# Kernel tuning notes

Measured on AMD Instinct MI355X. Metric: run time of the kernel, lower is better.

The kernel has to match this reference:

```python
import jax, jax.numpy as jnp
import numpy as np
import math

P_PARTICLES = 50
N_ITERS = 30
ROT_RANGE = math.radians(45.0)
TR_RANGE = 1.0
F_DE = 0.8
CR_DE = 0.9
SUB = 128


def axis_angle_to_rotation_matrix(v):
    # v: [..., 3] axis-angle -> [..., 3, 3] via Rodrigues formula
    theta = jnp.linalg.norm(v, axis=-1, keepdims=True)            # [..., 1]
    k = v / jnp.maximum(theta, 1e-8)
    kx, ky, kz = k[..., 0], k[..., 1], k[..., 2]
    zero = jnp.zeros_like(kx)
    K = jnp.stack([zero, -kz, ky,
                   kz, zero, -kx,
                   -ky, kx, zero], axis=-1).reshape(v.shape[:-1] + (3, 3))
    I = jnp.eye(3, dtype=v.dtype)
    s = jnp.sin(theta)[..., None]
    c = jnp.cos(theta)[..., None]
    R = I + s * K + (1.0 - c) * (K @ K)
    return jnp.where(theta[..., None] < 1e-8, I, R)


def _evaluate(src, tgt, pop):
    # src: [B,S,3] subsampled source, tgt: [B,S,3], pop: [B,P,6]
    R = axis_angle_to_rotation_matrix(pop[..., :3])               # [B,P,3,3]
    t = pop[..., 3:]                                              # [B,P,3]
    # transformed[b,p,n,k] = sum_j src[b,n,j] * R[b,p,k,j] + t[b,p,k]
    x = jnp.einsum('bnj,bpkj->bpnk', src, R) + t[:, :, None, :]   # [B,P,S,3]
    # squared-distance chamfer (symmetric, mean of nearest-neighbor dists)
    xn = jnp.sum(x * x, axis=-1)                                  # [B,P,S]
    yn = jnp.sum(tgt * tgt, axis=-1)                              # [B,S]
    cross = jnp.einsum('bpnd,bmd->bpnm', x, tgt)                  # [B,P,S,S]
    d2 = jnp.maximum(xn[..., None] + yn[:, None, None, :] - 2.0 * cross, 0.0)
    return d2.min(axis=-1).mean(axis=-1) + d2.min(axis=-2).mean(axis=-1)  # [B,P]


def setup_inputs() -> dict:
    key = jax.random.key(0)
    k1, k2 = jax.random.split(key)
    source = jax.random.normal(k1, (32, 16384, 3), dtype=jnp.float32)
    target = jax.random.normal(k2, (32, 16384, 3), dtype=jnp.float32)
    return {"source": source, "target": target}


def reference(source, target):
    B, N, _ = source.shape
    M = target.shape[1]
    P = P_PARTICLES
    key = jax.random.key(42)
    k0, k1, k2, k3, kloop = jax.random.split(key, 5)

    # subsample points for fitness evaluation (shared indices across batch)
    idx_s = jax.random.permutation(k0, N)[:SUB]
    idx_t = jax.random.permutation(k1, M)[:SUB]
    src = source[:, idx_s, :]                                     # [B,S,3]
    tgt = target[:, idx_t, :]                                     # [B,S,3]

    # init population: uniform axis-angle + translation; particle 0 = identity
    rot = jax.random.uniform(k2, (B, P, 3), minval=-ROT_RANGE, maxval=ROT_RANGE)
    tr = jax.random.uniform(k3, (B, P, 3), minval=-TR_RANGE, maxval=TR_RANGE)
    pop = jnp.concatenate([rot, tr], axis=-1).at[:, 0, :].set(0.0)
    fit = _evaluate(src, tgt, pop)                                # [B,P]

    dim_ids = jnp.arange(6)

    def step(carry, k):
        pop, fit = carry
        ka, kb, kc = jax.random.split(k, 3)
        # per-batch random permutations of particle indices (r1, r2, r3)
        perm_keys = jax.random.split(ka, 3 * B)
        perms = jax.vmap(lambda kk: jax.random.permutation(kk, P))(perm_keys)
        perms = perms.reshape(3, B, P)

        def gather(r):
            return jnp.take_along_axis(pop, r[..., None], axis=1)  # [B,P,6]

        x1, x2, x3 = gather(perms[0]), gather(perms[1]), gather(perms[2])
        mutant = x1 + F_DE * (x2 - x3)
        mutant = jnp.concatenate([
            jnp.clip(mutant[..., :3], -ROT_RANGE, ROT_RANGE),
            jnp.clip(mutant[..., 3:], -TR_RANGE, TR_RANGE),
        ], axis=-1)

        rmask = jax.random.uniform(kb, (B, P, 6)) < CR_DE
        j_rand = jax.random.randint(kc, (B, P), 0, 6)
        cross_mask = rmask | (dim_ids == j_rand[..., None])
        trial = jnp.where(cross_mask, mutant, pop)

        tfit = _evaluate(src, tgt, trial)
        improved = tfit < fit
        pop = jnp.where(improved[..., None], trial, pop)
        fit = jnp.where(improved, tfit, fit)
        return (pop, fit), None

    (pop, fit), _ = jax.lax.scan(step, (pop, fit), jax.random.split(kloop, N_ITERS))

    best_idx = jnp.argmin(fit, axis=1)                            # [B]
    best_pos = pop[jnp.arange(B), best_idx]                       # [B,6]
    R_best = axis_angle_to_rotation_matrix(best_pos[:, :3])       # [B,3,3]
    t_best = best_pos[:, 3:]                                      # [B,3]
    aligned = jnp.einsum('bnj,bkj->bnk', source, R_best) + t_best[:, None, :]
    return (R_best, t_best, aligned)
```

## Files before the change

kernel.cpp:

```cpp
#include <hip/hip_runtime.h>
#include <stdint.h>

struct U2 { unsigned a, b; };

__device__ __forceinline__ unsigned rotl32(unsigned v, int r) {
  return (v << r) | (v >> (32 - r));
}

__device__ __forceinline__ U2 tf(U2 k, unsigned x0, unsigned x1) {
  unsigned ks0 = k.a, ks1 = k.b, ks2 = k.a ^ k.b ^ 0x1BD11BDAu;
  x0 += ks0; x1 += ks1;
#define TFG(RA, RB, RC, RD, KA, KB, INC)                  \
  x0 += x1; x1 = rotl32(x1, RA); x1 ^= x0;                \
  x0 += x1; x1 = rotl32(x1, RB); x1 ^= x0;                \
  x0 += x1; x1 = rotl32(x1, RC); x1 ^= x0;                \
  x0 += x1; x1 = rotl32(x1, RD); x1 ^= x0;                \
  x0 += KA; x1 += KB + INC;
  TFG(13, 15, 26, 6, ks1, ks2, 1u)
  TFG(17, 29, 16, 24, ks2, ks0, 2u)
  TFG(13, 15, 26, 6, ks0, ks1, 3u)
  TFG(17, 29, 16, 24, ks1, ks2, 4u)
  TFG(13, 15, 26, 6, ks2, ks0, 5u)
#undef TFG
  U2 r; r.a = x0; r.b = x1; return r;
}

__device__ __forceinline__ U2 split_key(U2 key, int num, int j) {
  (void)num;
  return tf(key, 0u, (unsigned)j);
}
__device__ __forceinline__ unsigned random_bits(U2 key, int n, unsigned e) {
  (void)n;
  U2 r = tf(key, 0u, e);
  return r.a ^ r.b;
}

__device__ __forceinline__ U2 root_key() { U2 k; k.a = 0u; k.b = 42u; return k; }

__device__ __forceinline__ float jax_uniform(U2 key, int n, unsigned e,
                                             float minv, float maxv) {
  unsigned b = random_bits(key, n, e);
  float u = __uint_as_float((b >> 9) | 0x3f800000u) - 1.0f;
  float r = u * (maxv - minv) + minv;
  return fmaxf(minv, r);
}

#define ROTR 0.7853981633974483f
#define SENTINEL 0xFFFFFFFFu

__device__ __forceinline__ void compute_R(float vx, float vy, float vz,
                                          float R[3][3]) {
  float nsq = vx * vx + vy * vy + vz * vz;
  float theta = sqrtf(nsq);
  if (theta < 1e-8f) {
    R[0][0] = 1.f; R[0][1] = 0.f; R[0][2] = 0.f;
    R[1][0] = 0.f; R[1][1] = 1.f; R[1][2] = 0.f;
    R[2][0] = 0.f; R[2][1] = 0.f; R[2][2] = 1.f;
    return;
  }
  float m = fmaxf(theta, 1e-8f);
  float kx = vx / m, ky = vy / m, kz = vz / m;
  float s = sinf(theta), c = cosf(theta);
  float K[3][3] = {{0.f, -kz, ky}, {kz, 0.f, -kx}, {-ky, kx, 0.f}};
  float K2[3][3];
#pragma unroll
  for (int i = 0; i < 3; i++)
#pragma unroll
    for (int j = 0; j < 3; j++)
      K2[i][j] = fmaf(K[i][2], K[2][j], fmaf(K[i][1], K[1][j], K[i][0] * K[0][j]));
  float omc = 1.0f - c;
#pragma unroll
  for (int i = 0; i < 3; i++)
#pragma unroll
    for (int j = 0; j < 3; j++)
      R[i][j] = ((i == j) ? 1.0f : 0.0f) + s * K[i][j] + omc * K2[i][j];
}

__device__ __forceinline__ unsigned long long make_composite(int s, int i) {
  U2 root = root_key();
  U2 kp = split_key(root, 5, s >> 1);
  U2 key;
  if ((s & 1) == 0) {
    key = split_key(kp, 2, 1);
  } else {
    U2 kA = split_key(kp, 2, 0);
    key = split_key(kA, 2, 1);
  }
  unsigned rb = random_bits(key, 16384, (unsigned)i);
  return ((unsigned long long)rb << 32) | (unsigned)i;
}

__device__ __forceinline__ float gload(const float* p) {
  return __hip_atomic_load(const_cast<float*>(p), __ATOMIC_RELAXED,
                           __HIP_MEMORY_SCOPE_AGENT);
}
__device__ __forceinline__ void gstore(float* p, float v) {
  __hip_atomic_store(p, v, __ATOMIC_RELAXED, __HIP_MEMORY_SCOPE_AGENT);
}
__device__ __forceinline__ unsigned uload(const unsigned* p) {
  return __hip_atomic_load(const_cast<unsigned*>(p), __ATOMIC_RELAXED,
                           __HIP_MEMORY_SCOPE_AGENT);
}

__device__ __forceinline__ float poll_word(const float* p) {
  const unsigned* up = (const unsigned*)p;
  unsigned v = uload(up);
  while (v == SENTINEL) v = uload(up);
  return __uint_as_float(v);
}

__global__ __launch_bounds__(256) void hist_kernel(unsigned* __restrict__ hist) {
  int gid = blockIdx.x * 256 + threadIdx.x;
  int s = gid >> 14, i = gid & 16383;
  unsigned long long c = make_composite(s, i);
  unsigned bucket = (unsigned)(c >> 56);
  atomicAdd(&hist[s * 256 + bucket], 1u);
}

__global__ __launch_bounds__(256) void prefix_kernel(
    const unsigned* __restrict__ hist, unsigned* __restrict__ base,
    unsigned* __restrict__ cursor) {
  __shared__ unsigned h[4][256];
  int t = threadIdx.x;
#pragma unroll
  for (int s = 0; s < 4; s++) h[s][t] = hist[s * 256 + t];
  __syncthreads();
#pragma unroll
  for (int s = 0; s < 4; s++) {
    unsigned acc = 0;
    for (int j = 0; j < 256; j++) acc += (j < t) ? h[s][j] : 0u;
    base[s * 256 + t] = acc;
    cursor[s * 256 + t] = acc;
  }
}

__global__ __launch_bounds__(256) void scatterb_kernel(
    unsigned* __restrict__ cursor, unsigned long long* __restrict__ sorted) {
  int gid = blockIdx.x * 256 + threadIdx.x;
  int s = gid >> 14, i = gid & 16383;
  unsigned long long c = make_composite(s, i);
  unsigned bucket = (unsigned)(c >> 56);
  unsigned pos = atomicAdd(&cursor[s * 256 + bucket], 1u);
  sorted[(s << 14) + pos] = c;
}

__global__ __launch_bounds__(256) void rank_kernel(
    const unsigned long long* __restrict__ sorted,
    const unsigned* __restrict__ base, const unsigned* __restrict__ hist,
    unsigned* __restrict__ rank_all, unsigned* __restrict__ x1buf) {
  int gid = blockIdx.x * 256 + threadIdx.x;
  int s = gid >> 14, k = gid & 16383;
  unsigned long long c = sorted[(s << 14) + k];
  unsigned bucket = (unsigned)(c >> 56);
  unsigned b0 = base[s * 256 + bucket];
  unsigned cnt = hist[s * 256 + bucket];
  unsigned less = 0;
  for (unsigned j = 0; j < cnt; j++)
    less += (sorted[(s << 14) + b0 + j] < c) ? 1u : 0u;
  unsigned i = (unsigned)(c & 0xffffffffull);
  unsigned rank = b0 + less;
  if ((s & 1) == 0) x1buf[((s >> 1) << 14) + rank] = i;
  else              rank_all[(s << 14) + i] = rank;
}

__global__ __launch_bounds__(256) void idx_kernel(
    const unsigned* __restrict__ rank_all, const unsigned* __restrict__ x1buf,
    int* __restrict__ idx) {
  int gid = blockIdx.x * 256 + threadIdx.x;
  int perm = gid >> 14, i = gid & 16383;
  unsigned r = rank_all[((perm * 2 + 1) << 14) + i];
  if (r < 128u) idx[perm * 128 + (int)r] = (int)x1buf[(perm << 14) + i];
}

__global__ __launch_bounds__(128) void setupperm_kernel(
    const float* __restrict__ source, const float* __restrict__ target,
    const int* __restrict__ idx, float* __restrict__ src,
    float* __restrict__ tgt, float* __restrict__ yn,
    unsigned* __restrict__ packg) {
  int blk = blockIdx.x;
  int tid = threadIdx.x;
  if (blk < 32) {
    int b = blk;
    int is = idx[tid], it = idx[128 + tid];
#pragma unroll
    for (int d = 0; d < 3; d++)
      src[(b * 128 + tid) * 3 + d] = source[((size_t)b * 16384 + is) * 3 + d];
    float y0 = target[((size_t)b * 16384 + it) * 3 + 0];
    float y1 = target[((size_t)b * 16384 + it) * 3 + 1];
    float y2 = target[((size_t)b * 16384 + it) * 3 + 2];
    tgt[(b * 128 + tid) * 3 + 0] = y0;
    tgt[(b * 128 + tid) * 3 + 1] = y1;
    tgt[(b * 128 + tid) * 3 + 2] = y2;
    yn[b * 128 + tid] = y0 * y0 + y1 * y1 + y2 * y2;
    return;
  }
  int blk2 = blk - 32;
  int it = blk2 >> 5, b = blk2 & 31;
  __shared__ unsigned pbits[3][64];
  __shared__ int lperm[3][64];
  U2 root = root_key();
  U2 kloop = split_key(root, 5, 4);
  U2 kit = split_key(kloop, 30, it);
  U2 ka = split_key(kit, 3, 0);
  for (int e = tid; e < 150; e += 128) {
    int r = e / 50, q = e % 50;
    U2 pk = split_key(ka, 96, r * 32 + b);
    U2 sub = split_key(pk, 2, 1);
    pbits[r][q] = random_bits(sub, 50, (unsigned)q);
  }
  __syncthreads();
  for (int e = tid; e < 150; e += 128) {
    int r = e / 50, q = e % 50;
    unsigned bq = pbits[r][q];
    int cnt = 0;
    for (int j = 0; j < 50; j++) {
      unsigned bj = pbits[r][j];
      cnt += (bj < bq || (bj == bq && j < q)) ? 1 : 0;
    }
    lperm[r][cnt] = q;
  }
  __syncthreads();
  if (tid < 50) {
    int p = tid, bp = b * 50 + p;
    U2 kb = split_key(kit, 3, 1);
    U2 kc = split_key(kit, 3, 2);
    U2 kc1 = split_key(kc, 2, 0), kc2 = split_key(kc, 2, 1);
    unsigned hb = random_bits(kc1, 1600, (unsigned)bp);
    unsigned lb = random_bits(kc2, 1600, (unsigned)bp);
    int jr = (int)((((hb % 6u) * 4u) + (lb % 6u)) % 6u);
    unsigned mask = 0;
#pragma unroll
    for (int d = 0; d < 6; d++) {
      unsigned rb = random_bits(kb, 9600, (unsigned)(bp * 6 + d));
      float u = __uint_as_float((rb >> 9) | 0x3f800000u) - 1.0f;
      if ((u < 0.9f) || (d == jr)) mask |= (1u << d);
    }
    unsigned pack = (unsigned)lperm[0][p] | ((unsigned)lperm[1][p] << 6) |
                    ((unsigned)lperm[2][p] << 12) | (mask << 18);
    packg[(it * 32 + b) * 50 + p] = pack;
  }
}

__device__ __forceinline__ float eval_pose_core(
    float p0, float p1, float p2, float p3, float p4, float p5,
    float s0, float s1, float s2, int tid, const float4* syv, float4* xsv,
    float* rowpart, float* red1, float* red2) {
  float Rm[3][3];
  compute_R(p0, p1, p2, Rm);
  float x0 = fmaf(Rm[0][2], s2, fmaf(Rm[0][1], s1, Rm[0][0] * s0)) + p3;
  float x1 = fmaf(Rm[1][2], s2, fmaf(Rm[1][1], s1, Rm[1][0] * s0)) + p4;
  float x2 = fmaf(Rm[2][2], s2, fmaf(Rm[2][1], s1, Rm[2][0] * s0)) + p5;
  float xn = x0 * x0 + x1 * x1 + x2 * x2;
  xsv[tid] = make_float4(x0, x1, x2, xn);
  __syncthreads();
  int rg = tid & 31, cq = tid >> 5;
  float4 xr0 = xsv[4 * rg + 0];
  float4 xr1 = xsv[4 * rg + 1];
  float4 xr2 = xsv[4 * rg + 2];
  float4 xr3 = xsv[4 * rg + 3];
  float racc0 = 3.402823466e38f, racc1 = 3.402823466e38f;
  float racc2 = 3.402823466e38f, racc3 = 3.402823466e38f;
  float cacc[32];
#pragma unroll
  for (int cj = 0; cj < 32; cj++) {
    float4 y = syv[(cq << 5) + cj];
    float cr0 = fmaf(xr0.z, y.z, fmaf(xr0.y, y.y, xr0.x * y.x));
    float d0 = (xr0.w + y.w) - 2.0f * cr0; d0 = fmaxf(d0, 0.0f);
    float cr1 = fmaf(xr1.z, y.z, fmaf(xr1.y, y.y, xr1.x * y.x));
    float d1 = (xr1.w + y.w) - 2.0f * cr1; d1 = fmaxf(d1, 0.0f);
    float cr2 = fmaf(xr2.z, y.z, fmaf(xr2.y, y.y, xr2.x * y.x));
    float d2_ = (xr2.w + y.w) - 2.0f * cr2; d2_ = fmaxf(d2_, 0.0f);
    float cr3 = fmaf(xr3.z, y.z, fmaf(xr3.y, y.y, xr3.x * y.x));
    float d3 = (xr3.w + y.w) - 2.0f * cr3; d3 = fmaxf(d3, 0.0f);
    racc0 = fminf(racc0, d0); racc1 = fminf(racc1, d1);
    racc2 = fminf(racc2, d2_); racc3 = fminf(racc3, d3);
    cacc[cj] = fminf(fminf(d0, d1), fminf(d2_, d3));
  }
  rowpart[cq * 128 + 4 * rg + 0] = racc0;
  rowpart[cq * 128 + 4 * rg + 1] = racc1;
  rowpart[cq * 128 + 4 * rg + 2] = racc2;
  rowpart[cq * 128 + 4 * rg + 3] = racc3;
#pragma unroll
  for (int m = 16; m >= 1; m >>= 1) {
    bool hi = (rg & m) != 0;
#pragma unroll
    for (int j = 0; j < m; j++) {
      float lo_v = cacc[j], hi_v = cacc[j + m];
      float mine = hi ? hi_v : lo_v;
      float send = hi ? lo_v : hi_v;
      float recv = __shfl_xor(send, m, 64);
      cacc[j] = fminf(mine, recv);
    }
  }
  float colmin = cacc[0];
  __syncthreads();
  float rv = rowpart[tid];
  rv = fminf(rv, rowpart[128 + tid]);
  rv = fminf(rv, rowpart[256 + tid]);
  rv = fminf(rv, rowpart[384 + tid]);
  red1[tid] = rv;
  red2[tid] = colmin;
  __syncthreads();
  int l = tid & 63;
  float v1 = red1[l] + red1[l + 64];
  float v2 = red2[l] + red2[l + 64];
#pragma unroll
  for (int m = 32; m >= 1; m >>= 1) {
    v1 += __shfl_xor(v1, m, 64);
    v2 += __shfl_xor(v2, m, 64);
  }
  return v1 * 0.0078125f + v2 * 0.0078125f;
}

__device__ __forceinline__ float pop0_val(int b, int r, int d) {
  if (r == 0) return 0.0f;
  U2 root = root_key();
  unsigned ridx = (unsigned)((b * 50 + r) * 3 + (d % 3));
  if (d < 3) {
    U2 k2 = split_key(root, 5, 2);
    return jax_uniform(k2, 4800, ridx, -ROTR, ROTR);
  }
  U2 k3 = split_key(root, 5, 3);
  return jax_uniform(k3, 4800, ridx, -1.0f, 1.0f);
}

__global__ __launch_bounds__(128, 4) void de_loop_kernel(
    const float* __restrict__ srcb, const float* __restrict__ tgtb,
    const float* __restrict__ ynb, const unsigned* __restrict__ packg,
    float* __restrict__ estate, const float* __restrict__ source,
    float* __restrict__ out) {
  int blk = blockIdx.x;
  int b = blk / 50, p = blk % 50;
  int bp = blk;
  int tid = threadIdx.x;
  __shared__ float strial[8];
  __shared__ float pv4[4][6];
  __shared__ float4 syv[128];
  __shared__ float4 xsv[128];
  __shared__ float rowpart[512];
  __shared__ float red1[128];
  __shared__ float red2[128];
  __shared__ float fl[52];
  __shared__ float Rsh2[12];

  {
    float y0 = tgtb[(b * 128 + tid) * 3 + 0];
    float y1 = tgtb[(b * 128 + tid) * 3 + 1];
    float y2 = tgtb[(b * 128 + tid) * 3 + 2];
    syv[tid] = make_float4(y0, y1, y2, ynb[b * 128 + tid]);
  }
  float s0 = srcb[(b * 128 + tid) * 3 + 0];
  float s1 = srcb[(b * 128 + tid) * 3 + 1];
  float s2 = srcb[(b * 128 + tid) * 3 + 2];

  float own_f = 0.0f;
  float own_e = 0.0f;

  unsigned pack_next = packg[(0 * 32 + b) * 50 + p];

  for (int it = 0; it < 30; it++) {
    unsigned pack = pack_next;
    if (it < 29) pack_next = packg[((it + 1) * 32 + b) * 50 + p];
    int i1 = (int)(pack & 63u);
    int i2 = (int)((pack >> 6) & 63u);
    int i3 = (int)((pack >> 12) & 63u);
    unsigned mask = (pack >> 18) & 63u;

    if (it == 0) {
      if (tid < 24) {
        int u = tid / 6, d = tid % 6;
        int rows[4] = {p, i1, i2, i3};
        pv4[u][d] = pop0_val(b, rows[u], d);
      }
      __syncthreads();
      float f0 = eval_pose_core(pv4[0][0], pv4[0][1], pv4[0][2], pv4[0][3],
                                pv4[0][4], pv4[0][5],
                                s0, s1, s2, tid, syv, xsv, rowpart, red1, red2);
      if (tid < 6) {
        int d = tid;
        float mu = pv4[1][d] + 0.8f * (pv4[2][d] - pv4[3][d]);
        if (d < 3) mu = fminf(fmaxf(mu, -ROTR), ROTR);
        else       mu = fminf(fmaxf(mu, -1.0f), 1.0f);
        float pv = pv4[0][d];
        float tv = ((mask >> d) & 1u) ? mu : pv;
        strial[d] = tv;
      }
      __syncthreads();
      float tf0 = eval_pose_core(strial[0], strial[1], strial[2], strial[3],
                                 strial[4], strial[5],
                                 s0, s1, s2, tid, syv, xsv, rowpart, red1, red2);
      bool imp = tf0 < f0;
      own_f = imp ? tf0 : f0;
      if (tid < 6) own_e = imp ? strial[tid] : pv4[0][tid];
    } else {
      if (tid < 6) {
        int d = tid;
        const float* eb = &estate[((size_t)(it - 1) * 1600 + b * 50) * 8];
        const unsigned* pa = (const unsigned*)&eb[i1 * 8 + d];
        const unsigned* pb = (const unsigned*)&eb[i2 * 8 + d];
        const unsigned* pc = (const unsigned*)&eb[i3 * 8 + d];
        unsigned va = uload(pa), vb = uload(pb), vc = uload(pc);
        while (va == SENTINEL || vb == SENTINEL || vc == SENTINEL) {
          va = uload(pa); vb = uload(pb); vc = uload(pc);
        }
        float x1v = __uint_as_float(va);
        float x2v = __uint_as_float(vb);
        float x3v = __uint_as_float(vc);
        float mu = x1v + 0.8f * (x2v - x3v);
        if (d < 3) mu = fminf(fmaxf(mu, -ROTR), ROTR);
        else       mu = fminf(fmaxf(mu, -1.0f), 1.0f);
        float tv = ((mask >> d) & 1u) ? mu : own_e;
        strial[d] = tv;
      }
      __syncthreads();
      float tfv = eval_pose_core(strial[0], strial[1], strial[2], strial[3],
                                 strial[4], strial[5],
                                 s0, s1, s2, tid, syv, xsv, rowpart, red1, red2);
      bool imp = tfv < own_f;
      own_f = imp ? tfv : own_f;
      if (tid < 6) own_e = imp ? strial[tid] : own_e;
    }

    float* slot = &estate[((size_t)it * 1600 + bp) * 8];
    if (tid < 6)       gstore(&slot[tid], own_e);
    else if (tid == 6) gstore(&slot[6], own_f);
  }

  if (tid < 50) {
    fl[tid] = poll_word(&estate[((size_t)29 * 1600 + b * 50 + tid) * 8 + 6]);
  }
  __syncthreads();
  if (tid == 0) {
    int bi = 0;
    float best = fl[0];
    for (int q = 1; q < 50; q++)
      if (fl[q] < best) { best = fl[q]; bi = q; }
    const float* ep = &estate[((size_t)29 * 1600 + b * 50 + bi) * 8];
    float v[6];
#pragma unroll
    for (int d = 0; d < 6; d++) v[d] = poll_word(&ep[d]);
    float R[3][3];
    compute_R(v[0], v[1], v[2], R);
#pragma unroll
    for (int i = 0; i < 3; i++)
#pragma unroll
      for (int j = 0; j < 3; j++) Rsh2[i * 3 + j] = R[i][j];
    Rsh2[9] = v[3]; Rsh2[10] = v[4]; Rsh2[11] = v[5];
    if (p == 0) {
#pragma unroll
      for (int e = 0; e < 9; e++) out[b * 9 + e] = Rsh2[e];
      out[288 + b * 3 + 0] = v[3];
      out[288 + b * 3 + 1] = v[4];
      out[288 + b * 3 + 2] = v[5];
    }
  }
  __syncthreads();

  for (int k = p * 128 + tid; k < 16384; k += 6400) {
    size_t gid = (size_t)b * 16384 + k;
    float a0s = source[gid * 3 + 0];
    float a1s = source[gid * 3 + 1];
    float a2s = source[gid * 3 + 2];
    float a0 = fmaf(Rsh2[2], a2s, fmaf(Rsh2[1], a1s, Rsh2[0] * a0s)) + Rsh2[9];
    float a1 = fmaf(Rsh2[5], a2s, fmaf(Rsh2[4], a1s, Rsh2[3] * a0s)) + Rsh2[10];
    float a2 = fmaf(Rsh2[8], a2s, fmaf(Rsh2[7], a1s, Rsh2[6] * a0s)) + Rsh2[11];
    out[384 + gid * 3 + 0] = a0;
    out[384 + gid * 3 + 1] = a1;
    out[384 + gid * 3 + 2] = a2;
  }
}

extern "C" void kernel_launch(void* const* d_in, const int* in_sizes, int n_in,
                              void* d_out, int out_size, void* d_ws,
                              size_t ws_size, hipStream_t stream) {
  const float* source = (const float*)d_in[0];
  const float* target = (const float*)d_in[1];
  float* out = (float*)d_out;
  char* ws = (char*)d_ws;

  unsigned* packg    = (unsigned*)(ws + 0);
  float* srcb        = (float*)(ws + 192000);
  float* tgtb        = (float*)(ws + 241152);
  float* ynb         = (float*)(ws + 290304);
  int* idx           = (int*)(ws + 306688);
  unsigned* hist     = (unsigned*)(ws + 307712);
  unsigned* basep    = (unsigned*)(ws + 414208);
  unsigned* cursor   = (unsigned*)(ws + 418304);
  unsigned long long* sorted = (unsigned long long*)(ws + 422400);
  unsigned* rank_all = (unsigned*)(ws + 946688);
  unsigned* x1buf    = (unsigned*)(ws + 1208832);
  float* estate      = (float*)(ws + 422400);

  hipMemsetAsync(hist, 0, 4096, stream);
  hist_kernel<<<256, 256, 0, stream>>>(hist);
  prefix_kernel<<<1, 256, 0, stream>>>(hist, basep, cursor);
  scatterb_kernel<<<256, 256, 0, stream>>>(cursor, sorted);
  rank_kernel<<<256, 256, 0, stream>>>(sorted, basep, hist, rank_all, x1buf);
  idx_kernel<<<128, 256, 0, stream>>>(rank_all, x1buf, idx);
  hipMemsetAsync(estate, 0xFF, 1536000, stream);
  setupperm_kernel<<<992, 128, 0, stream>>>(source, target, idx, srcb, tgtb,
                                            ynb, packg);

  de_loop_kernel<<<1600, 128, 0, stream>>>(srcb, tgtb, ynb, packg, estate,
                                           source, out);
}
```

Measured before the change: 362.4 us.

## Pack chamfer inner loop for paired float ops, fold memset, add poll sleeps

```diff
diff --git a/kernel.cpp b/kernel.cpp
--- a/kernel.cpp
+++ b/kernel.cpp
@@ -48,6 +48,15 @@
 #define ROTR 0.7853981633974483f
 #define SENTINEL 0xFFFFFFFFu
 
+typedef float f2 __attribute__((ext_vector_type(2)));
+__device__ __forceinline__ f2 sp2(float s) { f2 v; v.x = s; v.y = s; return v; }
+__device__ __forceinline__ f2 fma2(f2 a, f2 b, f2 c) {
+  return __builtin_elementwise_fma(a, b, c);
+}
+__device__ __forceinline__ f2 max2(f2 a, f2 b) {
+  return __builtin_elementwise_max(a, b);
+}
+
 __device__ __forceinline__ void compute_R(float vx, float vy, float vz,
                                           float R[3][3]) {
   float nsq = vx * vx + vy * vy + vz * vz;
@@ -105,7 +114,10 @@
 __device__ __forceinline__ float poll_word(const float* p) {
   const unsigned* up = (const unsigned*)p;
   unsigned v = uload(up);
-  while (v == SENTINEL) v = uload(up);
+  while (v == SENTINEL) {
+    __builtin_amdgcn_s_sleep(1);
+    v = uload(up);
+  }
   return __uint_as_float(v);
 }
 
@@ -176,9 +188,11 @@
     const float* __restrict__ source, const float* __restrict__ target,
     const int* __restrict__ idx, float* __restrict__ src,
     float* __restrict__ tgt, float* __restrict__ yn,
-    unsigned* __restrict__ packg) {
+    unsigned* __restrict__ packg, unsigned* __restrict__ ewords) {
   int blk = blockIdx.x;
   int tid = threadIdx.x;
+  for (int i = blk * 128 + tid; i < 384000; i += 126976)
+    ewords[i] = SENTINEL;
   if (blk < 32) {
     int b = blk;
     int is = idx[tid], it = idx[128 + tid];
@@ -243,7 +257,7 @@
 
 __device__ __forceinline__ float eval_pose_core(
     float p0, float p1, float p2, float p3, float p4, float p5,
-    float s0, float s1, float s2, int tid, const float4* syv, float4* xsv,
+    float s0, float s1, float s2, int tid, const float4* syp, float4* xsv,
     float* rowpart, float* red1, float* red2) {
   float Rm[3][3];
   compute_R(p0, p1, p2, Rm);
@@ -262,19 +276,27 @@
   float racc2 = 3.402823466e38f, racc3 = 3.402823466e38f;
   float cacc[32];
 #pragma unroll
-  for (int cj = 0; cj < 32; cj++) {
-    float4 y = syv[(cq << 5) + cj];
-    float cr0 = fmaf(xr0.z, y.z, fmaf(xr0.y, y.y, xr0.x * y.x));
-    float d0 = (xr0.w + y.w) - 2.0f * cr0; d0 = fmaxf(d0, 0.0f);
-    float cr1 = fmaf(xr1.z, y.z, fmaf(xr1.y, y.y, xr1.x * y.x));
-    float d1 = (xr1.w + y.w) - 2.0f * cr1; d1 = fmaxf(d1, 0.0f);
-    float cr2 = fmaf(xr2.z, y.z, fmaf(xr2.y, y.y, xr2.x * y.x));
-    float d2_ = (xr2.w + y.w) - 2.0f * cr2; d2_ = fmaxf(d2_, 0.0f);
-    float cr3 = fmaf(xr3.z, y.z, fmaf(xr3.y, y.y, xr3.x * y.x));
-    float d3 = (xr3.w + y.w) - 2.0f * cr3; d3 = fmaxf(d3, 0.0f);
-    racc0 = fminf(racc0, d0); racc1 = fminf(racc1, d1);
-    racc2 = fminf(racc2, d2_); racc3 = fminf(racc3, d3);
-    cacc[cj] = fminf(fminf(d0, d1), fminf(d2_, d3));
+  for (int jj = 0; jj < 16; jj++) {
+    float4 A = syp[(cq << 5) + 2 * jj];
+    float4 B = syp[(cq << 5) + 2 * jj + 1];
+    f2 yx; yx.x = A.x; yx.y = A.y;
+    f2 yy; yy.x = A.z; yy.y = A.w;
+    f2 yz; yz.x = B.x; yz.y = B.y;
+    f2 yw; yw.x = B.z; yw.y = B.w;
+    f2 cr0 = fma2(sp2(xr0.z), yz, fma2(sp2(xr0.y), yy, sp2(xr0.x) * yx));
+    f2 d0 = (sp2(xr0.w) + yw) - 2.0f * cr0; d0 = max2(d0, sp2(0.0f));
+    f2 cr1 = fma2(sp2(xr1.z), yz, fma2(sp2(xr1.y), yy, sp2(xr1.x) * yx));
+    f2 d1 = (sp2(xr1.w) + yw) - 2.0f * cr1; d1 = max2(d1, sp2(0.0f));
+    f2 cr2 = fma2(sp2(xr2.z), yz, fma2(sp2(xr2.y), yy, sp2(xr2.x) * yx));
+    f2 d2_ = (sp2(xr2.w) + yw) - 2.0f * cr2; d2_ = max2(d2_, sp2(0.0f));
+    f2 cr3 = fma2(sp2(xr3.z), yz, fma2(sp2(xr3.y), yy, sp2(xr3.x) * yx));
+    f2 d3 = (sp2(xr3.w) + yw) - 2.0f * cr3; d3 = max2(d3, sp2(0.0f));
+    racc0 = fminf(fminf(racc0, d0.x), d0.y);
+    racc1 = fminf(fminf(racc1, d1.x), d1.y);
+    racc2 = fminf(fminf(racc2, d2_.x), d2_.y);
+    racc3 = fminf(fminf(racc3, d3.x), d3.y);
+    cacc[2 * jj]     = fminf(fminf(d0.x, d1.x), fminf(d2_.x, d3.x));
+    cacc[2 * jj + 1] = fminf(fminf(d0.y, d1.y), fminf(d2_.y, d3.y));
   }
   rowpart[cq * 128 + 4 * rg + 0] = racc0;
   rowpart[cq * 128 + 4 * rg + 1] = racc1;
@@ -335,7 +357,7 @@
   int tid = threadIdx.x;
   __shared__ float strial[8];
   __shared__ float pv4[4][6];
-  __shared__ float4 syv[128];
+  __shared__ float4 syp[128];
   __shared__ float4 xsv[128];
   __shared__ float rowpart[512];
   __shared__ float red1[128];
@@ -344,10 +366,18 @@
   __shared__ float Rsh2[12];
 
   {
-    float y0 = tgtb[(b * 128 + tid) * 3 + 0];
-    float y1 = tgtb[(b * 128 + tid) * 3 + 1];
-    float y2 = tgtb[(b * 128 + tid) * 3 + 2];
-    syv[tid] = make_float4(y0, y1, y2, ynb[b * 128 + tid]);
+    int e = tid;
+    int ecq = e >> 5, rem = e & 31, jj = rem >> 1, h = rem & 1;
+    int c0 = (ecq << 5) + 2 * jj, c1 = c0 + 1;
+    float a0, a1, b0, b1;
+    if (h == 0) {
+      a0 = tgtb[(b * 128 + c0) * 3 + 0]; a1 = tgtb[(b * 128 + c1) * 3 + 0];
+      b0 = tgtb[(b * 128 + c0) * 3 + 1]; b1 = tgtb[(b * 128 + c1) * 3 + 1];
+    } else {
+      a0 = tgtb[(b * 128 + c0) * 3 + 2]; a1 = tgtb[(b * 128 + c1) * 3 + 2];
+      b0 = ynb[b * 128 + c0];            b1 = ynb[b * 128 + c1];
+    }
+    syp[e] = make_float4(a0, a1, b0, b1);
   }
   float s0 = srcb[(b * 128 + tid) * 3 + 0];
   float s1 = srcb[(b * 128 + tid) * 3 + 1];
@@ -375,7 +405,7 @@
       __syncthreads();
       float f0 = eval_pose_core(pv4[0][0], pv4[0][1], pv4[0][2], pv4[0][3],
                                 pv4[0][4], pv4[0][5],
-                                s0, s1, s2, tid, syv, xsv, rowpart, red1, red2);
+                                s0, s1, s2, tid, syp, xsv, rowpart, red1, red2);
       if (tid < 6) {
         int d = tid;
         float mu = pv4[1][d] + 0.8f * (pv4[2][d] - pv4[3][d]);
@@ -388,7 +418,7 @@
       __syncthreads();
       float tf0 = eval_pose_core(strial[0], strial[1], strial[2], strial[3],
                                  strial[4], strial[5],
-                                 s0, s1, s2, tid, syv, xsv, rowpart, red1, red2);
+                                 s0, s1, s2, tid, syp, xsv, rowpart, red1, red2);
       bool imp = tf0 < f0;
       own_f = imp ? tf0 : f0;
       if (tid < 6) own_e = imp ? strial[tid] : pv4[0][tid];
@@ -401,6 +431,7 @@
         const unsigned* pc = (const unsigned*)&eb[i3 * 8 + d];
         unsigned va = uload(pa), vb = uload(pb), vc = uload(pc);
         while (va == SENTINEL || vb == SENTINEL || vc == SENTINEL) {
+          __builtin_amdgcn_s_sleep(1);
           va = uload(pa); vb = uload(pb); vc = uload(pc);
         }
         float x1v = __uint_as_float(va);
@@ -415,7 +446,7 @@
       __syncthreads();
       float tfv = eval_pose_core(strial[0], strial[1], strial[2], strial[3],
                                  strial[4], strial[5],
-                                 s0, s1, s2, tid, syv, xsv, rowpart, red1, red2);
+                                 s0, s1, s2, tid, syp, xsv, rowpart, red1, red2);
       bool imp = tfv < own_f;
       own_f = imp ? tfv : own_f;
       if (tid < 6) own_e = imp ? strial[tid] : own_e;
@@ -497,9 +528,8 @@
   scatterb_kernel<<<256, 256, 0, stream>>>(cursor, sorted);
   rank_kernel<<<256, 256, 0, stream>>>(sorted, basep, hist, rank_all, x1buf);
   idx_kernel<<<128, 256, 0, stream>>>(rank_all, x1buf, idx);
-  hipMemsetAsync(estate, 0xFF, 1536000, stream);
   setupperm_kernel<<<992, 128, 0, stream>>>(source, target, idx, srcb, tgtb,
-                                            ynb, packg);
+                                            ynb, packg, (unsigned*)estate);
 
   de_loop_kernel<<<1600, 128, 0, stream>>>(srcb, tgtb, ynb, packg, estate,
                                            source, out);
```

New measurement: 384.0 us. 1.06x slower.
